# Optimization experiments

Measured on AMD Instinct MI355X. Metric: run time of the kernel, lower is better.

## Reference

```python
import jax, jax.numpy as jnp
import numpy as np

D_MODEL = 1024
NUM_HEADS = 16
D_K = D_MODEL // NUM_HEADS
D_FF = 4096
EPS = 1e-5


def _layernorm(x, gamma, beta):
    mu = jnp.mean(x, axis=-1, keepdims=True)
    var = jnp.mean(jnp.square(x - mu), axis=-1, keepdims=True)
    return (x - mu) * jax.lax.rsqrt(var + EPS) * gamma + beta


def setup_inputs() -> dict:
    key = jax.random.key(0)
    ks = jax.random.split(key, 16)
    B, S = 4, 2048
    s_in = 1.0 / np.sqrt(D_MODEL)
    s_ff = 1.0 / np.sqrt(D_FF)
    inp = {
        "x": jax.random.normal(ks[0], (B, S, D_MODEL), jnp.float32),
        "src_mask": jnp.ones((B, 1, 1, S), jnp.int32),
        "w_q": jax.random.normal(ks[1], (D_MODEL, D_MODEL), jnp.float32) * s_in,
        "b_q": jnp.zeros((D_MODEL,), jnp.float32),
        "w_k": jax.random.normal(ks[2], (D_MODEL, D_MODEL), jnp.float32) * s_in,
        "b_k": jnp.zeros((D_MODEL,), jnp.float32),
        "w_v": jax.random.normal(ks[3], (D_MODEL, D_MODEL), jnp.float32) * s_in,
        "b_v": jnp.zeros((D_MODEL,), jnp.float32),
        "w_o": jax.random.normal(ks[4], (D_MODEL, D_MODEL), jnp.float32) * s_in,
        "b_o": jnp.zeros((D_MODEL,), jnp.float32),
        "w1": jax.random.normal(ks[5], (D_MODEL, D_FF), jnp.float32) * s_in,
        "b1": jnp.zeros((D_FF,), jnp.float32),
        "w2": jax.random.normal(ks[6], (D_FF, D_MODEL), jnp.float32) * s_ff,
        "b2": jnp.zeros((D_MODEL,), jnp.float32),
        "g1": jnp.ones((D_MODEL,), jnp.float32),
        "be1": jnp.zeros((D_MODEL,), jnp.float32),
        "g2": jnp.ones((D_MODEL,), jnp.float32),
        "be2": jnp.zeros((D_MODEL,), jnp.float32),
    }
    return inp


def reference(x, src_mask, w_q, b_q, w_k, b_k, w_v, b_v, w_o, b_o,
              w1, b1, w2, b2, g1, be1, g2, be2):
    B, S, _ = x.shape

    def split_heads(t):  # [B,S,D] -> [B,H,S,dk]
        return t.reshape(B, S, NUM_HEADS, D_K).transpose(0, 2, 1, 3)

    q = split_heads(x @ w_q + b_q)
    k = split_heads(x @ w_k + b_k)
    v = split_heads(x @ w_v + b_v)

    scores = jnp.einsum("bhqd,bhkd->bhqk", q, k) / np.sqrt(D_K)
    scores = jnp.where(src_mask == 0, -jnp.inf, scores)
    attn = jax.nn.softmax(scores, axis=-1)
    ctx = jnp.einsum("bhqk,bhkd->bhqd", attn, v)
    merged = ctx.transpose(0, 2, 1, 3).reshape(B, S, D_MODEL)
    attn_out = merged @ w_o + b_o

    h = _layernorm(x + attn_out, g1, be1)
    ff = jax.nn.relu(h @ w1 + b1) @ w2 + b2
    return _layernorm(h + ff, g2, be2)
```

## Files before the change

### kernel.cpp

```cpp
#include <hip/hip_runtime.h>

typedef unsigned short u16;
typedef __attribute__((ext_vector_type(4))) unsigned short u16x4;
typedef __attribute__((ext_vector_type(8))) short bf16x8;
typedef __attribute__((ext_vector_type(4))) float f32x4;

__device__ inline float bf2f(u16 u) {
  union { unsigned int i; float f; } v; v.i = ((unsigned int)u) << 16; return v.f;
}
__device__ inline u16 f2bf(float f) {
  union { float f; unsigned int i; } v; v.f = f;
  unsigned int r = v.i + 0x7fffu + ((v.i >> 16) & 1u);
  return (u16)(r >> 16);
}
__device__ inline unsigned int pack2bf(float lo, float hi) {
  union { float f; unsigned int i; } a, b; a.f = lo; b.f = hi;
  return __builtin_amdgcn_perm(b.i + 0x8000u, a.i + 0x8000u, 0x07060302u);
}

typedef const __attribute__((address_space(1))) unsigned int* gas_t;
typedef __attribute__((address_space(3))) unsigned int* las_t;
__device__ inline void gload_lds16(const u16* g, u16* l) {
  __builtin_amdgcn_global_load_lds((gas_t)(unsigned long long)(const void*)g,
                                   (las_t)(unsigned int)(unsigned long long)(void*)l,
                                   16, 0, 0);
}

__global__ __launch_bounds__(256) void cvt_bf16(const float* __restrict__ src,
                                                u16* __restrict__ dst, int n) {
  int i = (blockIdx.x * 256 + threadIdx.x) * 4;
  if (i >= n) return;
  float4 v = *(const float4*)(src + i);
  u16x4 o;
  o.x = f2bf(v.x); o.y = f2bf(v.y); o.z = f2bf(v.z); o.w = f2bf(v.w);
  *(u16x4*)(dst + i) = o;
}

__global__ __launch_bounds__(256) void concat3(const float* __restrict__ a,
                                               const float* __restrict__ b,
                                               const float* __restrict__ c,
                                               float* __restrict__ o, int n) {
  int i = blockIdx.x * 256 + threadIdx.x;
  if (i >= n) return;
  o[i] = a[i]; o[n + i] = b[i]; o[2 * n + i] = c[i];
}

__global__ __launch_bounds__(256) void transpose_f32_bf16(const float* __restrict__ src,
                                                          u16* __restrict__ dst,
                                                          int R, int C) {
  __shared__ u16 tile[32][33];
  int tx = threadIdx.x & 31, ty = threadIdx.x >> 5;
  int c0 = blockIdx.x * 32, r0 = blockIdx.y * 32;
  #pragma unroll
  for (int i = ty; i < 32; i += 8)
    tile[i][tx] = f2bf(src[(size_t)(r0 + i) * C + c0 + tx]);
  __syncthreads();
  #pragma unroll
  for (int i = ty; i < 32; i += 8)
    dst[(size_t)(c0 + i) * R + r0 + tx] = tile[tx][i];
}

__global__ __launch_bounds__(256) void transpose_v(const u16* __restrict__ src,
                                                   u16* __restrict__ VT,
                                                   int B, int S, int H, int RS, int CO) {
  __shared__ u16 tile[32][33];
  int tx = threadIdx.x & 31, ty = threadIdx.x >> 5;
  int s0 = blockIdx.x * 32, d0 = blockIdx.y * 32;
  int bh = blockIdx.z;
  int b = bh / H, h = bh % H;
  #pragma unroll
  for (int i = ty; i < 32; i += 8)
    tile[i][tx] = src[(size_t)(b * S + s0 + i) * RS + CO + h * 64 + d0 + tx];
  __syncthreads();
  #pragma unroll
  for (int i = ty; i < 32; i += 8)
    VT[((size_t)bh * 64 + d0 + i) * S + s0 + tx] = tile[tx][i];
}

__global__ __launch_bounds__(256) void gemm_bt(const u16* __restrict__ A,
                                               const u16* __restrict__ Bt,
                                               const float* __restrict__ bias,
                                               u16* __restrict__ C,
                                               int M, int N, int K, int relu) {
  __shared__ u16 As[128 * 32];
  __shared__ u16 Bs[128 * 32];
  const int tid = threadIdx.x;
  const int lane = tid & 63, wid = tid >> 6;
  const int lr = lane & 15, quad = lane >> 4;
  const int wm = (wid >> 1) * 64, wn = (wid & 1) * 64;
  const int m0 = blockIdx.y * 128, n0 = blockIdx.x * 128;
  const int lrow = lane >> 2;
  const int lcol = (lane & 3) * 8;

  f32x4 acc[4][4];
  const f32x4 zero = {0.f, 0.f, 0.f, 0.f};
  #pragma unroll
  for (int mt = 0; mt < 4; ++mt)
    #pragma unroll
    for (int nt = 0; nt < 4; ++nt) acc[mt][nt] = zero;

  for (int k0 = 0; k0 < K; k0 += 32) {
    #pragma unroll
    for (int it = 0; it < 2; ++it) {
      int rbase = wid * 32 + it * 16;
      gload_lds16(A + (size_t)(m0 + rbase + lrow) * K + k0 + lcol, &As[rbase * 32]);
      gload_lds16(Bt + (size_t)(n0 + rbase + lrow) * K + k0 + lcol, &Bs[rbase * 32]);
    }
    __syncthreads();
    bf16x8 af[4], bfr[4];
    #pragma unroll
    for (int mt = 0; mt < 4; ++mt)
      af[mt] = *(const bf16x8*)(&As[(wm + mt * 16 + lr) * 32 + quad * 8]);
    #pragma unroll
    for (int nt = 0; nt < 4; ++nt)
      bfr[nt] = *(const bf16x8*)(&Bs[(wn + nt * 16 + lr) * 32 + quad * 8]);
    #pragma unroll
    for (int mt = 0; mt < 4; ++mt)
      #pragma unroll
      for (int nt = 0; nt < 4; ++nt)
        acc[mt][nt] = __builtin_amdgcn_mfma_f32_16x16x32_bf16(af[mt], bfr[nt], acc[mt][nt], 0, 0, 0);
    __syncthreads();
  }

  #pragma unroll
  for (int nt = 0; nt < 4; ++nt) {
    int n = n0 + wn + nt * 16 + lr;
    float bv = bias[n];
    #pragma unroll
    for (int mt = 0; mt < 4; ++mt) {
      #pragma unroll
      for (int i = 0; i < 4; ++i) {
        int m = m0 + wm + mt * 16 + quad * 4 + i;
        float v = acc[mt][nt][i] + bv;
        if (relu) v = fmaxf(v, 0.f);
        C[(size_t)m * N + n] = f2bf(v);
      }
    }
  }
}

__global__ __launch_bounds__(256) void flash_attn(const u16* __restrict__ Qp,
                                                  const u16* __restrict__ Kp,
                                                  const u16* __restrict__ VT,
                                                  const int* __restrict__ mask,
                                                  u16* __restrict__ ctx,
                                                  int B, int S, int H, int QSTR) {
  __shared__ u16 kt_lds[64 * 72];
  __shared__ u16 vt_lds[64 * 72];
  __shared__ u16 p_lds[4 * 16 * 72];
  __shared__ float msk_lds[64];
  const int tid = threadIdx.x;
  const int lane = tid & 63, wid = tid >> 6;
  const int lr = lane & 15, quad = lane >> 4;
  const int bh = blockIdx.y;
  const int b = bh / H, h = bh % H;
  const int q0 = blockIdx.x * 64;
  const u16* vt_base = VT + (size_t)bh * 64 * S;
  const float SC = 0.125f * 1.44269504089f;

  bf16x8 qf[2];
  {
    int qm = q0 + wid * 16 + lr;
    const u16* qptr = Qp + (size_t)(b * S + qm) * QSTR + h * 64;
    qf[0] = *(const bf16x8*)(qptr + quad * 8);
    qf[1] = *(const bf16x8*)(qptr + 32 + quad * 8);
  }

  float m_i = -1e30f, l_i = 0.f;
  float O[4][4];
  #pragma unroll
  for (int nt = 0; nt < 4; ++nt)
    #pragma unroll
    for (int i = 0; i < 4; ++i) O[nt][i] = 0.f;

  u16* pw = &p_lds[wid * 16 * 72];

  for (int kt = 0; kt < S; kt += 64) {
    #pragma unroll
    for (int it = 0; it < 2; ++it) {
      int c = tid + it * 256;
      int r = c >> 3;
      int cc = (c & 7) * 8;
      uint4 kv = *(const uint4*)(Kp + (size_t)(b * S + kt + r) * QSTR + h * 64 + cc);
      *(uint4*)(&kt_lds[r * 72 + cc]) = kv;
      uint4 vv = *(const uint4*)(vt_base + (size_t)r * S + kt + cc);
      *(uint4*)(&vt_lds[r * 72 + cc]) = vv;
    }
    if (tid < 64) msk_lds[tid] = mask[b * S + kt + tid] ? 0.f : -1e30f;
    __syncthreads();

    float s[4][4];
    #pragma unroll
    for (int st = 0; st < 4; ++st) {
      f32x4 c = {0.f, 0.f, 0.f, 0.f};
      bf16x8 kf0 = *(const bf16x8*)(&kt_lds[(st * 16 + lr) * 72 + quad * 8]);
      bf16x8 kf1 = *(const bf16x8*)(&kt_lds[(st * 16 + lr) * 72 + 32 + quad * 8]);
      c = __builtin_amdgcn_mfma_f32_16x16x32_bf16(kf0, qf[0], c, 0, 0, 0);
      c = __builtin_amdgcn_mfma_f32_16x16x32_bf16(kf1, qf[1], c, 0, 0, 0);
      float4 mv = *(const float4*)(&msk_lds[st * 16 + quad * 4]);
      s[st][0] = c[0] * SC + mv.x;
      s[st][1] = c[1] * SC + mv.y;
      s[st][2] = c[2] * SC + mv.z;
      s[st][3] = c[3] * SC + mv.w;
    }

    float tmax = s[0][0];
    #pragma unroll
    for (int st = 0; st < 4; ++st)
      #pragma unroll
      for (int i = 0; i < 4; ++i) tmax = fmaxf(tmax, s[st][i]);
    tmax = fmaxf(tmax, __shfl_xor(tmax, 16, 64));
    tmax = fmaxf(tmax, __shfl_xor(tmax, 32, 64));
    float mn = fmaxf(m_i, tmax);
    float al = exp2f(m_i - mn);
    m_i = mn;
    float rs = 0.f;
    #pragma unroll
    for (int st = 0; st < 4; ++st)
      #pragma unroll
      for (int i = 0; i < 4; ++i) {
        float p = exp2f(s[st][i] - mn);
        s[st][i] = p; rs += p;
      }
    rs += __shfl_xor(rs, 16, 64);
    rs += __shfl_xor(rs, 32, 64);
    l_i = l_i * al + rs;

    #pragma unroll
    for (int st = 0; st < 4; ++st) {
      uint2 pk;
      pk.x = pack2bf(s[st][0], s[st][1]);
      pk.y = pack2bf(s[st][2], s[st][3]);
      *(uint2*)(&pw[lr * 72 + st * 16 + quad * 4]) = pk;
    }

    bf16x8 pf0 = *(const bf16x8*)(&pw[lr * 72 + quad * 8]);
    bf16x8 pf1 = *(const bf16x8*)(&pw[lr * 72 + 32 + quad * 8]);
    #pragma unroll
    for (int nt = 0; nt < 4; ++nt) {
      f32x4 c;
      c[0] = O[nt][0] * al; c[1] = O[nt][1] * al;
      c[2] = O[nt][2] * al; c[3] = O[nt][3] * al;
      bf16x8 vf0 = *(const bf16x8*)(&vt_lds[(nt * 16 + lr) * 72 + quad * 8]);
      bf16x8 vf1 = *(const bf16x8*)(&vt_lds[(nt * 16 + lr) * 72 + 32 + quad * 8]);
      c = __builtin_amdgcn_mfma_f32_16x16x32_bf16(vf0, pf0, c, 0, 0, 0);
      c = __builtin_amdgcn_mfma_f32_16x16x32_bf16(vf1, pf1, c, 0, 0, 0);
      O[nt][0] = c[0]; O[nt][1] = c[1]; O[nt][2] = c[2]; O[nt][3] = c[3];
    }
    __syncthreads();
  }

  float linv = 1.f / fmaxf(l_i, 1e-30f);
  int q = q0 + wid * 16 + lr;
  u16* op = ctx + (size_t)(b * S + q) * (H * 64) + h * 64;
  #pragma unroll
  for (int nt = 0; nt < 4; ++nt) {
    u16x4 o;
    o.x = f2bf(O[nt][0] * linv); o.y = f2bf(O[nt][1] * linv);
    o.z = f2bf(O[nt][2] * linv); o.w = f2bf(O[nt][3] * linv);
    *(u16x4*)(op + nt * 16 + quad * 4) = o;
  }
}

__device__ inline float block_reduce_sum(float v, float* sbuf) {
  #pragma unroll
  for (int m = 1; m < 64; m <<= 1) v += __shfl_xor(v, m, 64);
  int w = threadIdx.x >> 6;
  if ((threadIdx.x & 63) == 0) sbuf[w] = v;
  __syncthreads();
  v = sbuf[0] + sbuf[1] + sbuf[2] + sbuf[3];
  __syncthreads();
  return v;
}

__global__ __launch_bounds__(256) void add_ln(const float* __restrict__ a32,
                                              const u16* __restrict__ a16,
                                              const u16* __restrict__ b,
                                              const float* __restrict__ g,
                                              const float* __restrict__ be,
                                              u16* __restrict__ out16,
                                              float* __restrict__ out32, int D) {
  __shared__ float sbuf[4];
  int row = blockIdx.x;
  size_t base = (size_t)row * D;
  int i = threadIdx.x * 4;
  float v[4];
  {
    u16x4 bv = *(const u16x4*)(b + base + i);
    if (a32) {
      float4 av = *(const float4*)(a32 + base + i);
      v[0] = av.x + bf2f(bv.x); v[1] = av.y + bf2f(bv.y);
      v[2] = av.z + bf2f(bv.z); v[3] = av.w + bf2f(bv.w);
    } else {
      u16x4 av = *(const u16x4*)(a16 + base + i);
      v[0] = bf2f(av.x) + bf2f(bv.x); v[1] = bf2f(av.y) + bf2f(bv.y);
      v[2] = bf2f(av.z) + bf2f(bv.z); v[3] = bf2f(av.w) + bf2f(bv.w);
    }
  }
  float sum = v[0] + v[1] + v[2] + v[3];
  sum = block_reduce_sum(sum, sbuf);
  float mean = sum / (float)D;
  float var = 0.f;
  #pragma unroll
  for (int j = 0; j < 4; ++j) { float d = v[j] - mean; var += d * d; }
  var = block_reduce_sum(var, sbuf);
  float rstd = rsqrtf(var / (float)D + 1e-5f);
  float4 gv = *(const float4*)(g + i);
  float4 bev = *(const float4*)(be + i);
  float o0 = (v[0] - mean) * rstd * gv.x + bev.x;
  float o1 = (v[1] - mean) * rstd * gv.y + bev.y;
  float o2 = (v[2] - mean) * rstd * gv.z + bev.z;
  float o3 = (v[3] - mean) * rstd * gv.w + bev.w;
  if (out32) {
    float4 o = {o0, o1, o2, o3};
    *(float4*)(out32 + base + i) = o;
  } else {
    u16x4 o;
    o.x = f2bf(o0); o.y = f2bf(o1); o.z = f2bf(o2); o.w = f2bf(o3);
    *(u16x4*)(out16 + base + i) = o;
  }
}

extern "C" void kernel_launch(void* const* d_in, const int* in_sizes, int n_in,
                              void* d_out, int out_size, void* d_ws, size_t ws_size,
                              hipStream_t stream) {
  (void)in_sizes; (void)n_in; (void)out_size; (void)ws_size;
  const float* x   = (const float*)d_in[0];
  const int* mask  = (const int*)d_in[1];
  const float* wq  = (const float*)d_in[2];
  const float* bq  = (const float*)d_in[3];
  const float* wk  = (const float*)d_in[4];
  const float* bk  = (const float*)d_in[5];
  const float* wv  = (const float*)d_in[6];
  const float* bv  = (const float*)d_in[7];
  const float* wo  = (const float*)d_in[8];
  const float* bo  = (const float*)d_in[9];
  const float* w1  = (const float*)d_in[10];
  const float* b1  = (const float*)d_in[11];
  const float* w2  = (const float*)d_in[12];
  const float* b2  = (const float*)d_in[13];
  const float* g1  = (const float*)d_in[14];
  const float* be1 = (const float*)d_in[15];
  const float* g2  = (const float*)d_in[16];
  const float* be2 = (const float*)d_in[17];

  const int B = 4, S = 2048, D = 1024, H = 16, DFF = 4096;
  const int D3 = 3 * D;
  const size_t TOK = (size_t)B * S;
  const size_t TD = TOK * D;

  u16* ws   = (u16*)d_ws;
  u16* QKVp = ws;
  u16* xb   = ws + 3 * TD;
  u16* VT   = xb;
  u16* CTX  = ws + 4 * TD;
  u16* ATT  = ws + 5 * TD;
  u16* Hb   = ws + 6 * TD;
  u16* QKVT = ws + 7 * TD;
  u16* WOT  = QKVT + 3 * (size_t)D * D;
  u16* W1T  = WOT + (size_t)D * D;
  u16* FF1  = ws;
  u16* FF2  = ATT;
  u16* W2T  = QKVT;
  float* biasc = (float*)CTX;

  dim3 blk(256);

  cvt_bf16<<<dim3((unsigned)(TD / (256 * 4))), blk, 0, stream>>>(x, xb, (int)TD);
  concat3<<<dim3(4), blk, 0, stream>>>(bq, bk, bv, biasc, D);

  transpose_f32_bf16<<<dim3(D / 32, D / 32), blk, 0, stream>>>(wq, QKVT, D, D);
  transpose_f32_bf16<<<dim3(D / 32, D / 32), blk, 0, stream>>>(wk, QKVT + (size_t)D * D, D, D);
  transpose_f32_bf16<<<dim3(D / 32, D / 32), blk, 0, stream>>>(wv, QKVT + 2 * (size_t)D * D, D, D);
  transpose_f32_bf16<<<dim3(D / 32, D / 32), blk, 0, stream>>>(wo, WOT, D, D);
  transpose_f32_bf16<<<dim3(DFF / 32, D / 32), blk, 0, stream>>>(w1, W1T, D, DFF);

  gemm_bt<<<dim3(D3 / 128, TOK / 128), blk, 0, stream>>>(xb, QKVT, biasc, QKVp, (int)TOK, D3, D, 0);

  transpose_v<<<dim3(S / 32, 2, B * H), blk, 0, stream>>>(QKVp, VT, B, S, H, D3, 2 * D);

  flash_attn<<<dim3(S / 64, B * H), blk, 0, stream>>>(QKVp, QKVp + D, VT, mask, CTX, B, S, H, D3);

  gemm_bt<<<dim3(D / 128, TOK / 128), blk, 0, stream>>>(CTX, WOT, bo, ATT, (int)TOK, D, D, 0);

  transpose_f32_bf16<<<dim3(D / 32, DFF / 32), blk, 0, stream>>>(w2, W2T, DFF, D);

  add_ln<<<dim3((unsigned)TOK), blk, 0, stream>>>(x, (const u16*)nullptr, ATT, g1, be1,
                                                  Hb, (float*)nullptr, D);

  gemm_bt<<<dim3(DFF / 128, TOK / 128), blk, 0, stream>>>(Hb, W1T, b1, FF1, (int)TOK, DFF, D, 1);
  gemm_bt<<<dim3(D / 128, TOK / 128), blk, 0, stream>>>(FF1, W2T, b2, FF2, (int)TOK, D, DFF, 0);

  add_ln<<<dim3((unsigned)TOK), blk, 0, stream>>>((const float*)nullptr, Hb, FF2, g2, be2,
                                                  (u16*)nullptr, (float*)d_out, D);
}
```

Before: 664.3 us.

## Vectorize GEMM epilogue stores and use direct global-to-LDS loads in attention

The GEMM swaps its MFMA operand order so each lane holds four consecutive output columns. The epilogue can then load bias as float4 and write packed 8-byte bf16 stores instead of scattered 2-byte stores. The flash attention kernel now loads K/V tiles with global_load_lds into an unpadded, split-half LDS layout, bypassing registers. This layout may add LDS bank conflicts, and the output conversion switches to the cheaper pack2bf rounding.

```diff
diff --git a/kernel.cpp b/kernel.cpp
--- a/kernel.cpp
+++ b/kernel.cpp
@@ -118,23 +118,32 @@
     for (int mt = 0; mt < 4; ++mt)
       #pragma unroll
       for (int nt = 0; nt < 4; ++nt)
-        acc[mt][nt] = __builtin_amdgcn_mfma_f32_16x16x32_bf16(af[mt], bfr[nt], acc[mt][nt], 0, 0, 0);
+        acc[mt][nt] = __builtin_amdgcn_mfma_f32_16x16x32_bf16(bfr[nt], af[mt], acc[mt][nt], 0, 0, 0);
     __syncthreads();
   }
 
-  #pragma unroll
-  for (int nt = 0; nt < 4; ++nt) {
-    int n = n0 + wn + nt * 16 + lr;
-    float bv = bias[n];
-    #pragma unroll
-    for (int mt = 0; mt < 4; ++mt) {
-      #pragma unroll
-      for (int i = 0; i < 4; ++i) {
-        int m = m0 + wm + mt * 16 + quad * 4 + i;
-        float v = acc[mt][nt][i] + bv;
-        if (relu) v = fmaxf(v, 0.f);
-        C[(size_t)m * N + n] = f2bf(v);
+  float4 bvec[4];
+  #pragma unroll
+  for (int nt = 0; nt < 4; ++nt)
+    bvec[nt] = *(const float4*)(bias + n0 + wn + nt * 16 + quad * 4);
+  #pragma unroll
+  for (int mt = 0; mt < 4; ++mt) {
+    int m = m0 + wm + mt * 16 + lr;
+    u16* crow = C + (size_t)m * N + n0 + wn;
+    #pragma unroll
+    for (int nt = 0; nt < 4; ++nt) {
+      float v0 = acc[mt][nt][0] + bvec[nt].x;
+      float v1 = acc[mt][nt][1] + bvec[nt].y;
+      float v2 = acc[mt][nt][2] + bvec[nt].z;
+      float v3 = acc[mt][nt][3] + bvec[nt].w;
+      if (relu) {
+        v0 = fmaxf(v0, 0.f); v1 = fmaxf(v1, 0.f);
+        v2 = fmaxf(v2, 0.f); v3 = fmaxf(v3, 0.f);
       }
+      uint2 pk;
+      pk.x = pack2bf(v0, v1);
+      pk.y = pack2bf(v2, v3);
+      *(uint2*)(crow + nt * 16 + quad * 4) = pk;
     }
   }
 }
@@ -145,13 +154,15 @@
                                                   const int* __restrict__ mask,
                                                   u16* __restrict__ ctx,
                                                   int B, int S, int H, int QSTR) {
-  __shared__ u16 kt_lds[64 * 72];
-  __shared__ u16 vt_lds[64 * 72];
+  __shared__ u16 kt_lds[2 * 64 * 32];
+  __shared__ u16 vt_lds[2 * 64 * 32];
   __shared__ u16 p_lds[4 * 16 * 72];
   __shared__ float msk_lds[64];
   const int tid = threadIdx.x;
   const int lane = tid & 63, wid = tid >> 6;
   const int lr = lane & 15, quad = lane >> 4;
+  const int srow = lane >> 2;
+  const int scol = (lane & 3) * 8;
   const int bh = blockIdx.y;
   const int b = bh / H, h = bh % H;
   const int q0 = blockIdx.x * 64;
@@ -177,14 +188,11 @@
 
   for (int kt = 0; kt < S; kt += 64) {
     #pragma unroll
-    for (int it = 0; it < 2; ++it) {
-      int c = tid + it * 256;
-      int r = c >> 3;
-      int cc = (c & 7) * 8;
-      uint4 kv = *(const uint4*)(Kp + (size_t)(b * S + kt + r) * QSTR + h * 64 + cc);
-      *(uint4*)(&kt_lds[r * 72 + cc]) = kv;
-      uint4 vv = *(const uint4*)(vt_base + (size_t)r * S + kt + cc);
-      *(uint4*)(&vt_lds[r * 72 + cc]) = vv;
+    for (int ch = 0; ch < 2; ++ch) {
+      gload_lds16(Kp + (size_t)(b * S + kt + wid * 16 + srow) * QSTR + h * 64 + ch * 32 + scol,
+                  &kt_lds[ch * 2048 + wid * 16 * 32]);
+      gload_lds16(vt_base + (size_t)(wid * 16 + srow) * S + kt + ch * 32 + scol,
+                  &vt_lds[ch * 2048 + wid * 16 * 32]);
     }
     if (tid < 64) msk_lds[tid] = mask[b * S + kt + tid] ? 0.f : -1e30f;
     __syncthreads();
@@ -193,8 +201,8 @@
     #pragma unroll
     for (int st = 0; st < 4; ++st) {
       f32x4 c = {0.f, 0.f, 0.f, 0.f};
-      bf16x8 kf0 = *(const bf16x8*)(&kt_lds[(st * 16 + lr) * 72 + quad * 8]);
-      bf16x8 kf1 = *(const bf16x8*)(&kt_lds[(st * 16 + lr) * 72 + 32 + quad * 8]);
+      bf16x8 kf0 = *(const bf16x8*)(&kt_lds[(st * 16 + lr) * 32 + quad * 8]);
+      bf16x8 kf1 = *(const bf16x8*)(&kt_lds[2048 + (st * 16 + lr) * 32 + quad * 8]);
       c = __builtin_amdgcn_mfma_f32_16x16x32_bf16(kf0, qf[0], c, 0, 0, 0);
       c = __builtin_amdgcn_mfma_f32_16x16x32_bf16(kf1, qf[1], c, 0, 0, 0);
       float4 mv = *(const float4*)(&msk_lds[st * 16 + quad * 4]);
@@ -241,8 +249,8 @@
       f32x4 c;
       c[0] = O[nt][0] * al; c[1] = O[nt][1] * al;
       c[2] = O[nt][2] * al; c[3] = O[nt][3] * al;
-      bf16x8 vf0 = *(const bf16x8*)(&vt_lds[(nt * 16 + lr) * 72 + quad * 8]);
-      bf16x8 vf1 = *(const bf16x8*)(&vt_lds[(nt * 16 + lr) * 72 + 32 + quad * 8]);
+      bf16x8 vf0 = *(const bf16x8*)(&vt_lds[(nt * 16 + lr) * 32 + quad * 8]);
+      bf16x8 vf1 = *(const bf16x8*)(&vt_lds[2048 + (nt * 16 + lr) * 32 + quad * 8]);
       c = __builtin_amdgcn_mfma_f32_16x16x32_bf16(vf0, pf0, c, 0, 0, 0);
       c = __builtin_amdgcn_mfma_f32_16x16x32_bf16(vf1, pf1, c, 0, 0, 0);
       O[nt][0] = c[0]; O[nt][1] = c[1]; O[nt][2] = c[2]; O[nt][3] = c[3];
@@ -255,10 +263,10 @@
   u16* op = ctx + (size_t)(b * S + q) * (H * 64) + h * 64;
   #pragma unroll
   for (int nt = 0; nt < 4; ++nt) {
-    u16x4 o;
-    o.x = f2bf(O[nt][0] * linv); o.y = f2bf(O[nt][1] * linv);
-    o.z = f2bf(O[nt][2] * linv); o.w = f2bf(O[nt][3] * linv);
-    *(u16x4*)(op + nt * 16 + quad * 4) = o;
+    uint2 pk;
+    pk.x = pack2bf(O[nt][0] * linv, O[nt][1] * linv);
+    pk.y = pack2bf(O[nt][2] * linv, O[nt][3] * linv);
+    *(uint2*)(op + nt * 16 + quad * 4) = pk;
   }
 }
 
```

Result: slower. 701.4 us (+5.6%).
